# Optimization experiments

Measured on AMD Instinct MI355X. Metric: run time of the kernel, lower is better.

Reference implementation:

```python
import jax, jax.numpy as jnp
import numpy as np
from jax import lax

B, T, FEAT = 8, 512, 128
D_MODEL, D_STATE, D_INNER, DT_RANK = 128, 16, 256, 8
N_LAYERS, NUM_CLASSES = 10, 35
FLAT = 64 * (FEAT // 4)  # 2048


def setup_inputs():
    keys = iter(jax.random.split(jax.random.key(0), 48))
    def nrm(shape, s=0.05):
        return jax.random.normal(next(keys), shape, jnp.float32) * s
    inp = {}
    inp['x'] = jax.random.normal(next(keys), (B, T, FEAT), jnp.float32)
    inp['lengths'] = jax.random.randint(next(keys), (B,), 0, T)
    inp['conv_w1'] = nrm((32, 1, 3, 3)); inp['conv_b1'] = nrm((32,))
    inp['bn1_s'] = 1.0 + nrm((32,)); inp['bn1_b'] = nrm((32,))
    inp['conv_w2'] = nrm((32, 32, 3, 3)); inp['conv_b2'] = nrm((32,))
    inp['bn2_s'] = 1.0 + nrm((32,)); inp['bn2_b'] = nrm((32,))
    inp['conv_w3'] = nrm((64, 32, 3, 3)); inp['conv_b3'] = nrm((64,))
    inp['bn3_s'] = 1.0 + nrm((64,)); inp['bn3_b'] = nrm((64,))
    inp['conv_w4'] = nrm((64, 64, 3, 3)); inp['conv_b4'] = nrm((64,))
    inp['bn4_s'] = 1.0 + nrm((64,)); inp['bn4_b'] = nrm((64,))
    inp['proj_w'] = nrm((D_MODEL, FLAT), 0.02); inp['proj_b'] = nrm((D_MODEL,))
    inp['proj_ln_s'] = jnp.ones((D_MODEL,)); inp['proj_ln_b'] = jnp.zeros((D_MODEL,))
    L = N_LAYERS
    inp['blk_ln_s'] = jnp.ones((L, D_MODEL)); inp['blk_ln_b'] = jnp.zeros((L, D_MODEL))
    inp['in_w'] = nrm((L, 2 * D_INNER, D_MODEL))
    inp['cw'] = nrm((L, D_INNER, 4)); inp['cb'] = nrm((L, D_INNER))
    inp['xp_w'] = nrm((L, DT_RANK + 2 * D_STATE, D_INNER))
    inp['dt_w'] = nrm((L, D_INNER, DT_RANK))
    inp['dt_b'] = nrm((L, D_INNER)) - 4.0  # softplus(-4) ~ 0.018: realistic small dt
    inp['A_log'] = jnp.tile(jnp.log(jnp.arange(1, D_STATE + 1, dtype=jnp.float32))[None, None, :], (L, D_INNER, 1))
    inp['Dp'] = jnp.ones((L, D_INNER))
    inp['out_w'] = nrm((L, D_MODEL, D_INNER))
    inp['pre_ln_s'] = jnp.ones((D_MODEL,)); inp['pre_ln_b'] = jnp.zeros((D_MODEL,))
    inp['cls_w1'] = nrm((D_MODEL // 2, D_MODEL)); inp['cls_b1'] = nrm((D_MODEL // 2,))
    inp['cls_w2'] = nrm((NUM_CLASSES, D_MODEL // 2)); inp['cls_b2'] = nrm((NUM_CLASSES,))
    return inp


def _ln(x, s, b):
    m = jnp.mean(x, -1, keepdims=True)
    v = jnp.mean((x - m) ** 2, -1, keepdims=True)
    return (x - m) * lax.rsqrt(v + 1e-5) * s + b


def _conv2d(x, w, b):
    y = lax.conv_general_dilated(x, w, (1, 1), 'SAME', dimension_numbers=('NCHW', 'OIHW', 'NCHW'))
    return y + b[None, :, None, None]


def _bn(x, s, b):  # eval-mode BatchNorm folded to per-channel affine
    return x * s[None, :, None, None] + b[None, :, None, None]


def _pool(x, kh, kw):
    return lax.reduce_window(x, -jnp.inf, lax.max, (1, 1, kh, kw), (1, 1, kh, kw), 'VALID')


def _mamba(x, in_w, cw, cb, xp_w, dt_w, dt_b, A_log, Dp, out_w):
    bb = x.shape[0]
    xz = jnp.einsum('btd,ed->bte', x, in_w)                  # [B,T,2*d_inner]
    xm, z = jnp.split(xz, 2, axis=-1)
    # causal depthwise conv1d (torch pads both sides by 3 then truncates to T == left-pad 3)
    xc = lax.conv_general_dilated(xm.transpose(0, 2, 1), cw[:, None, :], (1,), [(3, 0)],
                                  dimension_numbers=('NCH', 'OIH', 'NCH'), feature_group_count=D_INNER)
    xc = jax.nn.silu(xc + cb[None, :, None]).transpose(0, 2, 1)  # [B,T,d_inner]
    dbc = jnp.einsum('btd,ed->bte', xc, xp_w)
    dt, Bm, Cm = jnp.split(dbc, [DT_RANK, DT_RANK + D_STATE], axis=-1)
    dt = jax.nn.softplus(jnp.einsum('btr,dr->btd', dt, dt_w) + dt_b)  # [B,T,d_inner]
    A = -jnp.exp(A_log)                                      # [d_inner,d_state]
    dA = jnp.exp(dt[..., None] * A)                          # [B,T,d,n]
    dBu = (dt * xc)[..., None] * Bm[:, :, None, :]           # [B,T,d,n]
    def step(h, inp):
        dA_t, dBu_t, C_t = inp
        h = dA_t * h + dBu_t
        return h, jnp.einsum('bdn,bn->bd', h, C_t)
    h0 = jnp.zeros((bb, D_INNER, D_STATE), x.dtype)
    _, ys = lax.scan(step, h0, (dA.transpose(1, 0, 2, 3), dBu.transpose(1, 0, 2, 3), Cm.transpose(1, 0, 2)))
    y = ys.transpose(1, 0, 2) + Dp * xc
    y = y * jax.nn.silu(z)
    return jnp.einsum('btd,ed->bte', y, out_w)


def _forward(x, lengths, conv_w1, conv_b1, bn1_s, bn1_b, conv_w2, conv_b2, bn2_s, bn2_b,
             conv_w3, conv_b3, bn3_s, bn3_b, conv_w4, conv_b4, bn4_s, bn4_b,
             proj_w, proj_b, proj_ln_s, proj_ln_b, blk_ln_s, blk_ln_b,
             in_w, cw, cb, xp_w, dt_w, dt_b, A_log, Dp, out_w,
             pre_ln_s, pre_ln_b, cls_w1, cls_b1, cls_w2, cls_b2):
    h = x.transpose(0, 2, 1)[:, None]                        # [B,1,F,T]
    h = jax.nn.silu(_bn(_conv2d(h, conv_w1, conv_b1), bn1_s, bn1_b))
    h = jax.nn.silu(_bn(_conv2d(h, conv_w2, conv_b2), bn2_s, bn2_b))
    h = _pool(h, 2, 2)
    h = jax.nn.silu(_bn(_conv2d(h, conv_w3, conv_b3), bn3_s, bn3_b))
    h = jax.nn.silu(_bn(_conv2d(h, conv_w4, conv_b4), bn4_s, bn4_b))
    h = _pool(h, 2, 1)                                       # [B,64,F/4,T/2]
    h = h.transpose(0, 3, 1, 2).reshape(h.shape[0], h.shape[3], -1)  # [B,T',64*F/4]
    h = jax.nn.silu(_ln(jnp.einsum('btf,df->btd', h, proj_w) + proj_b, proj_ln_s, proj_ln_b))
    for i in range(N_LAYERS):
        h = h + _mamba(_ln(h, blk_ln_s[i], blk_ln_b[i]), in_w[i], cw[i], cb[i], xp_w[i],
                       dt_w[i], dt_b[i], A_log[i], Dp[i], out_w[i])
    h = _ln(h, pre_ln_s, pre_ln_b)
    t_lens = jnp.clip(lengths // 2, 1)
    mask = (jnp.arange(h.shape[1])[None, :] < t_lens[:, None]).astype(h.dtype)[..., None]
    pooled = (h * mask).sum(1) / jnp.clip(mask.sum(1), 1.0)
    c = jax.nn.silu(jnp.einsum('bd,hd->bh', pooled, cls_w1) + cls_b1)
    return jnp.einsum('bh,ch->bc', c, cls_w2) + cls_b2


def reference(x, lengths, conv_w1, conv_b1, bn1_s, bn1_b, conv_w2, conv_b2, bn2_s, bn2_b,
              conv_w3, conv_b3, bn3_s, bn3_b, conv_w4, conv_b4, bn4_s, bn4_b,
              proj_w, proj_b, proj_ln_s, proj_ln_b, blk_ln_s, blk_ln_b,
              in_w, cw, cb, xp_w, dt_w, dt_b, A_log, Dp, out_w,
              pre_ln_s, pre_ln_b, cls_w1, cls_b1, cls_w2, cls_b2):
    return _forward(x, lengths, conv_w1, conv_b1, bn1_s, bn1_b, conv_w2, conv_b2, bn2_s, bn2_b,
                    conv_w3, conv_b3, bn3_s, bn3_b, conv_w4, conv_b4, bn4_s, bn4_b,
                    proj_w, proj_b, proj_ln_s, proj_ln_b, blk_ln_s, blk_ln_b,
                    in_w, cw, cb, xp_w, dt_w, dt_b, A_log, Dp, out_w,
                    pre_ln_s, pre_ln_b, cls_w1, cls_b1, cls_w2, cls_b2)
```

## Files before the change

kernel.cpp:

```cpp
#include <hip/hip_runtime.h>
#include <math.h>

#define B_ 8
#define T_ 512
#define FEAT_ 128
#define TP 256
#define DM 128
#define DI 256
#define DS 16
#define DTR 8
#define NL 10

__device__ __forceinline__ float fsilu(float x){ return x / (1.f + __expf(-x)); }
__device__ __forceinline__ float fsoftplus(float x){ return (x > 20.f) ? x : log1pf(__expf(x)); }

template<int CTRL>
__device__ __forceinline__ float dpp_ror(float x){
  int v = __builtin_amdgcn_update_dpp(0, __float_as_int(x), CTRL, 0xF, 0xF, false);
  return __int_as_float(v);
}
__device__ __forceinline__ float rsum16(float x){
  x += dpp_ror<0x121>(x);
  x += dpp_ror<0x122>(x);
  x += dpp_ror<0x124>(x);
  x += dpp_ror<0x128>(x);
  return x;
}

__global__ void k_transpose_x(const float* __restrict__ x, float* __restrict__ xT){
  int idx = blockIdx.x*256 + threadIdx.x;
  if(idx >= B_*FEAT_*T_) return;
  int t = idx % T_; int f = (idx/T_) % FEAT_; int b = idx/(T_*FEAT_);
  xT[idx] = x[((size_t)b*T_ + t)*FEAT_ + f];
}

__device__ __forceinline__ void wt_one(const float* __restrict__ w, float* __restrict__ o,
                                       int idx, int CO, int CIN){
  int k = idx % 9; int ci = (idx/9) % CIN; int co = idx/(9*CIN);
  o[((size_t)(ci*(CO>>3) + (co>>3)))*72 + (co&7)*9 + k] = w[idx];
}
__global__ void k_wt_all(const float* __restrict__ w1, const float* __restrict__ w2,
                         const float* __restrict__ w3, const float* __restrict__ w4,
                         float* __restrict__ o1, float* __restrict__ o2,
                         float* __restrict__ o3, float* __restrict__ o4){
  int idx = blockIdx.x*256 + threadIdx.x;
  if(idx < 288){ wt_one(w1, o1, idx, 32, 1); return; }
  idx -= 288;
  if(idx < 9216){ wt_one(w2, o2, idx, 32, 32); return; }
  idx -= 9216;
  if(idx < 18432){ wt_one(w3, o3, idx, 64, 32); return; }
  idx -= 18432;
  if(idx < 36864){ wt_one(w4, o4, idx, 64, 64); return; }
}

template<int CIN, int CO, int CPW, int CIG, int COG>
__global__ __launch_bounds__(256) void k_conv_t4(const float* __restrict__ in,
     const float* __restrict__ wt, const float* __restrict__ cb,
     const float* __restrict__ bs, const float* __restrict__ bb,
     float* __restrict__ out, int H, int W){
  constexpr int NS = CO/CPW;
  __shared__ __align__(16) float tile[CIG*360];
  int tid = threadIdx.x;
  int lane = tid & 63;
  int wav = __builtin_amdgcn_readfirstlane(tid >> 6);
  int wpr = W >> 4, hpr = H >> 4;
  int idx = blockIdx.x;
  int cog = idx % COG; idx /= COG;
  int tj = idx % wpr; idx /= wpr;
  int ti = idx % hpr; int b = idx / hpr;
  int i0 = ti*16, j0 = tj*16;
  int r = lane & 15, cg = lane >> 4;
  int wslot = cog*4 + wav;
  const float* wbase = wt + (size_t)wslot*72;
  float acc[CPW][4] = {};
  for(int cig = 0; cig < CIN; cig += CIG){
    __syncthreads();
    for(int u = tid; u < CIG*324; u += 256){
      int ci = u / 324; int rem = u - ci*324; int rr = rem / 18; int cc = rem - rr*18;
      int gi = i0 - 1 + rr, gj = j0 - 1 + cc;
      float v = 0.f;
      if(gi >= 0 && gi < H && gj >= 0 && gj < W)
        v = in[((size_t)(b*CIN + cig + ci)*H + gi)*W + gj];
      tile[ci*360 + rr*20 + cc] = v;
    }
    __syncthreads();
    for(int ci = 0; ci < CIG; ci++){
      const float4* wp4 = (const float4*)(wbase + (size_t)(cig+ci)*(NS*72));
      float4 w4q[18];
      #pragma unroll
      for(int q=0;q<18;q++) w4q[q] = wp4[q];
      const float* wf = (const float*)w4q;
      #pragma unroll
      for(int kh=0;kh<3;kh++){
        float4 a = *(const float4*)&tile[ci*360 + (r+kh)*20 + cg*4];
        float4 bv = *(const float4*)&tile[ci*360 + (r+kh)*20 + cg*4 + 4];
        float v[6] = {a.x,a.y,a.z,a.w,bv.x,bv.y};
        #pragma unroll
        for(int co=0;co<CPW;co++){
          #pragma unroll
          for(int kw=0;kw<3;kw++){
            float wv = wf[co*9 + kh*3 + kw];
            #pragma unroll
            for(int u2=0;u2<4;u2++)
              acc[co][u2] = fmaf(wv, v[kw+u2], acc[co][u2]);
          }
        }
      }
    }
  }
  int i = i0 + r;
  #pragma unroll
  for(int co=0; co<CPW; co++){
    int c = cog*(4*CPW) + wav*CPW + co;
    float s = bs[c], bias = cb[c]*s + bb[c];
    float4 o;
    o.x = fsilu(acc[co][0]*s + bias);
    o.y = fsilu(acc[co][1]*s + bias);
    o.z = fsilu(acc[co][2]*s + bias);
    o.w = fsilu(acc[co][3]*s + bias);
    *(float4*)&out[((size_t)(b*CO + c)*H + i)*W + j0 + cg*4] = o;
  }
}

__global__ void k_pool2x2(const float* __restrict__ in, float* __restrict__ out,
                          int C, int Hi, int Wi){
  int Ho = Hi>>1, Wo = Wi>>1;
  int total = B_*C*Ho*Wo;
  int idx = blockIdx.x*256 + threadIdx.x;
  if(idx >= total) return;
  int j = idx % Wo; int i = (idx/Wo)%Ho; int c = (idx/(Wo*Ho))%C; int b = idx/(Wo*Ho*C);
  const float* p = in + (((size_t)(b*C+c)*Hi + 2*i)*Wi + 2*j);
  out[idx] = fmaxf(fmaxf(p[0], p[1]), fmaxf(p[Wi], p[Wi+1]));
}

__global__ __launch_bounds__(256) void k_proj(const float* __restrict__ R0,
    const float* __restrict__ W, float* __restrict__ pbuf){
  __shared__ __align__(16) float As[16][33];
  __shared__ __align__(16) float Ws[16][68];
  int tid = threadIdx.x;
  int n0 = blockIdx.x*64, m0 = blockIdx.y*32;
  int kc = blockIdx.z;
  int b = m0 >> 8;
  int t_base = m0 & 255;
  int tx = tid&15, ty = tid>>4;
  float acc[2][4] = {};
  for(int k0=0; k0<256; k0+=16){
    int kg0 = kc*256 + k0;
    if(tid < 128){
      int row = tid>>2, cq = (tid&3)*4;
      #pragma unroll
      for(int c2=0;c2<4;c2++){
        int k = kg0 + cq + c2;
        int c = k>>5, hh = k&31;
        const float* p = R0 + (((size_t)(b*64+c)*64 + 2*hh)*256 + t_base + row);
        As[cq+c2][row] = fmaxf(p[0], p[256]);
      }
    } else {
      int u = tid - 128; int n = u>>1, cq = (u&1)*8;
      const float* wp = W + (size_t)(n0+n)*2048 + kg0 + cq;
      float4 v0 = *(const float4*)wp, v1 = *(const float4*)(wp+4);
      Ws[cq+0][n]=v0.x; Ws[cq+1][n]=v0.y; Ws[cq+2][n]=v0.z; Ws[cq+3][n]=v0.w;
      Ws[cq+4][n]=v1.x; Ws[cq+5][n]=v1.y; Ws[cq+6][n]=v1.z; Ws[cq+7][n]=v1.w;
    }
    __syncthreads();
    #pragma unroll
    for(int kk=0;kk<16;kk++){
      float a0 = As[kk][ty*2+0];
      float a1 = As[kk][ty*2+1];
      float4 w4 = *(const float4*)&Ws[kk][tx*4];
      float wv4[4] = {w4.x,w4.y,w4.z,w4.w};
      #pragma unroll
      for(int j=0;j<4;j++){
        acc[0][j] = fmaf(a0, wv4[j], acc[0][j]);
        acc[1][j] = fmaf(a1, wv4[j], acc[1][j]);
      }
    }
    __syncthreads();
  }
  float* pb = pbuf + (size_t)kc*2048*DM;
  #pragma unroll
  for(int iu=0;iu<2;iu++){
    int m = m0 + ty*2 + iu;
    #pragma unroll
    for(int j=0;j<4;j++){
      int n = n0 + tx*4 + j;
      pb[(size_t)m*DM + n] = acc[iu][j];
    }
  }
}

__global__ void k_lnp(const float* __restrict__ pbuf, const float* __restrict__ bias,
                      const float* __restrict__ g, const float* __restrict__ b,
                      float* __restrict__ out){
  int row = blockIdx.x;
  int t = threadIdx.x;
  float v0 = bias[t], v1 = bias[t+64];
  #pragma unroll
  for(int kc=0;kc<8;kc++){
    const float* p = pbuf + ((size_t)kc*2048 + row)*DM;
    v0 += p[t]; v1 += p[t+64];
  }
  float s = v0 + v1;
  #pragma unroll
  for(int m=32;m>=1;m>>=1) s += __shfl_xor(s, m);
  float mean = s * (1.f/128.f);
  float e0 = v0-mean, e1 = v1-mean;
  float q = e0*e0 + e1*e1;
  #pragma unroll
  for(int m=32;m>=1;m>>=1) q += __shfl_xor(q, m);
  float inv = rsqrtf(q*(1.f/128.f) + 1e-5f);
  float o0 = fsilu(e0*inv*g[t] + b[t]);
  float o1 = fsilu(e1*inv*g[t+64] + b[t+64]);
  float* po = out + (size_t)row*DM;
  po[t] = o0; po[t+64] = o1;
}

template<int SILU>
__global__ void k_ln(const float* __restrict__ in, const float* __restrict__ g,
                     const float* __restrict__ b, float* __restrict__ out){
  int row = blockIdx.x;
  int t = threadIdx.x;
  const float* p = in + (size_t)row*DM;
  float v0 = p[t], v1 = p[t+64];
  float s = v0 + v1;
  #pragma unroll
  for(int m=32;m>=1;m>>=1) s += __shfl_xor(s, m);
  float mean = s * (1.f/128.f);
  float e0 = v0-mean, e1 = v1-mean;
  float q = e0*e0 + e1*e1;
  #pragma unroll
  for(int m=32;m>=1;m>>=1) q += __shfl_xor(q, m);
  float inv = rsqrtf(q*(1.f/128.f) + 1e-5f);
  float o0 = e0*inv*g[t] + b[t];
  float o1 = e1*inv*g[t+64] + b[t+64];
  if(SILU){ o0 = fsilu(o0); o1 = fsilu(o1); }
  float* po = out + (size_t)row*DM;
  po[t] = o0; po[t+64] = o1;
}

__global__ __launch_bounds__(256) void k_lnxz(const float* __restrict__ hbuf,
    const float* __restrict__ g, const float* __restrict__ bb,
    const float* __restrict__ W, float* __restrict__ out){
  __shared__ __align__(16) float lns[32][132];
  __shared__ __align__(16) float Ws[16][68];
  int tid = threadIdx.x;
  int n0 = blockIdx.x*64, m0 = blockIdx.y*32;
  for(int u=tid; u<1024; u+=256){
    int row = u>>5, c4 = (u&31)*4;
    float4 v = *(const float4*)(hbuf + (size_t)(m0+row)*DM + c4);
    lns[row][c4] = v.x; lns[row][c4+1] = v.y; lns[row][c4+2] = v.z; lns[row][c4+3] = v.w;
  }
  __syncthreads();
  {
    int lane = tid & 63, wv = tid >> 6;
    for(int rr = wv; rr < 32; rr += 4){
      float v0 = lns[rr][lane], v1 = lns[rr][lane+64];
      float s = v0+v1;
      #pragma unroll
      for(int mm=32;mm>=1;mm>>=1) s += __shfl_xor(s,mm);
      float mean = s*(1.f/128.f);
      float e0 = v0-mean, e1 = v1-mean;
      float q = e0*e0+e1*e1;
      #pragma unroll
      for(int mm=32;mm>=1;mm>>=1) q += __shfl_xor(q,mm);
      float inv = rsqrtf(q*(1.f/128.f)+1e-5f);
      lns[rr][lane]    = e0*inv*g[lane] + bb[lane];
      lns[rr][lane+64] = e1*inv*g[lane+64] + bb[lane+64];
    }
  }
  __syncthreads();
  int tx = tid&15, ty = tid>>4;
  float acc[2][4] = {};
  for(int k0=0;k0<128;k0+=16){
    {
      int n = tid>>2, c4 = (tid&3)*4;
      float4 v = *(const float4*)(W + (size_t)(n0+n)*DM + k0 + c4);
      Ws[c4+0][n]=v.x; Ws[c4+1][n]=v.y; Ws[c4+2][n]=v.z; Ws[c4+3][n]=v.w;
    }
    __syncthreads();
    #pragma unroll
    for(int kk=0;kk<16;kk++){
      float a0 = lns[ty*2+0][k0+kk];
      float a1 = lns[ty*2+1][k0+kk];
      float4 w4 = *(const float4*)&Ws[kk][tx*4];
      float wv4[4] = {w4.x,w4.y,w4.z,w4.w};
      #pragma unroll
      for(int j=0;j<4;j++){
        acc[0][j] = fmaf(a0, wv4[j], acc[0][j]);
        acc[1][j] = fmaf(a1, wv4[j], acc[1][j]);
      }
    }
    __syncthreads();
  }
  #pragma unroll
  for(int iu=0;iu<2;iu++){
    int m = m0 + ty*2 + iu;
    float* po = out + (size_t)m*512 + n0 + tx*4;
    #pragma unroll
    for(int j=0;j<4;j++) po[j] = acc[iu][j];
  }
}

__global__ __launch_bounds__(256) void k_xproj8(const float* __restrict__ xz,
    const float* __restrict__ cw, const float* __restrict__ cb,
    const float* __restrict__ xpw, const float* __restrict__ dtw,
    const float* __restrict__ dtb_, float* __restrict__ xc_g,
    float* __restrict__ dbc_g, float* __restrict__ dt_g){
  __shared__ float xzs[11][64];
  __shared__ float As[64][9];
  __shared__ float Wp[64][41];
  __shared__ float dtin[8][9];
  __shared__ float dtw_s[256][9];
  int tid = threadIdx.x;
  int row0 = blockIdx.x*8; int b = row0 >> 8; int t0 = row0 & 255;
  int rA = tid & 7, cgA = tid >> 3;
  int dlC = tid & 63, rqC = tid >> 6;
  float acc0 = 0.f, acc1 = 0.f;
  for(int ch=0; ch<4; ch++){
    int d0 = ch*64;
    __syncthreads();
    for(int u=tid; u<11*64; u+=256){
      int rr = u>>6, dl = u&63;
      int t = t0 + rr - 3;
      xzs[rr][dl] = (t >= 0) ? xz[((size_t)(b*TP)+t)*512 + d0 + dl] : 0.f;
    }
    for(int u=tid; u<40*64; u+=256){
      int nn = u>>6, dk = u&63;
      Wp[dk][nn] = xpw[(size_t)nn*DI + d0 + dk];
    }
    __syncthreads();
    {
      float cw0 = cw[(d0+dlC)*4+0], cw1 = cw[(d0+dlC)*4+1];
      float cw2 = cw[(d0+dlC)*4+2], cw3 = cw[(d0+dlC)*4+3];
      float cbv = cb[d0+dlC];
      #pragma unroll
      for(int i=0;i<2;i++){
        int rr = rqC*2 + i;
        float a = cbv;
        a = fmaf(cw0, xzs[rr+0][dlC], a);
        a = fmaf(cw1, xzs[rr+1][dlC], a);
        a = fmaf(cw2, xzs[rr+2][dlC], a);
        a = fmaf(cw3, xzs[rr+3][dlC], a);
        float v = fsilu(a);
        As[dlC][rr] = v;
        xc_g[((size_t)row0 + rr)*DI + d0 + dlC] = v;
      }
    }
    __syncthreads();
    for(int dk=0; dk<64; dk++){
      float a = As[dk][rA];
      acc0 = fmaf(a, Wp[dk][cgA], acc0);
      if(cgA < 8) acc1 = fmaf(a, Wp[dk][cgA+32], acc1);
    }
  }
  if(cgA < 8){
    dtin[rA][cgA] = acc0;
    dbc_g[((size_t)row0 + rA)*40 + cgA + 32] = acc1;
  } else {
    dbc_g[((size_t)row0 + rA)*40 + cgA] = acc0;
  }
  for(int u=tid; u<256*8; u+=256) dtw_s[u>>3][u&7] = dtw[u];
  __syncthreads();
  {
    int d = tid;
    float bias = dtb_[d];
    float w8[8];
    #pragma unroll
    for(int k=0;k<8;k++) w8[k] = dtw_s[d][k];
    #pragma unroll
    for(int r2=0;r2<8;r2++){
      float a = bias;
      #pragma unroll
      for(int k=0;k<8;k++) a = fmaf(dtin[r2][k], w8[k], a);
      dt_g[((size_t)row0 + r2)*DI + d] = fsoftplus(a);
    }
  }
}

__global__ __launch_bounds__(1024) void k_scan4(const float* __restrict__ dtb,
      const float* __restrict__ xc, const float* __restrict__ xz,
      const float* __restrict__ dbc, const float* __restrict__ A_log,
      const float* __restrict__ Dp, float* __restrict__ y){
  __shared__ float dt_s[TP][8], xc_s[TP][8];
  __shared__ float Bs[TP][16], Cs[TP][16];
  __shared__ float Eb[8][128], Pb[8][128];
  int tid = threadIdx.x;
  int c = tid >> 7, gl = (tid >> 4) & 7, n = tid & 15;
  int dblk = blockIdx.x & 31, b = blockIdx.x >> 5;
  int d0 = dblk*8;
  size_t rbase = (size_t)b*TP;
  for(int u=tid; u<TP*8; u+=1024){
    int tt = u>>3, gg = u&7;
    size_t r = rbase + tt;
    dt_s[tt][gg] = dtb[r*DI + d0 + gg];
    xc_s[tt][gg] = xc [r*DI + d0 + gg];
  }
  for(int u=tid; u<TP*16; u+=1024){
    int tt = u>>4, nn = u&15;
    size_t r = rbase + tt;
    Bs[tt][nn] = dbc[r*40 + 8  + nn];
    Cs[tt][nn] = dbc[r*40 + 24 + nn];
  }
  __syncthreads();
  int d = d0 + gl;
  float An = -__expf(A_log[d*DS + n]);
  float h = 0.f, dtsum = 0.f;
  int tA = c*32;
  float hc[32], ev[32];
  #pragma unroll
  for(int i=0;i<32;i++){
    int t = tA + i;
    float dtv = dt_s[t][gl];
    dtsum += dtv;
    float e = __expf(dtv*An);
    ev[i] = e;
    h = fmaf(e, h, dtv*xc_s[t][gl]*Bs[t][n]);
    hc[i] = h*Cs[t][n];
  }
  Eb[c][gl*16+n] = h;
  Pb[c][gl*16+n] = __expf(An*dtsum);
  __syncthreads();
  float g = 0.f;
  for(int cp=0; cp<c; cp++)
    g = fmaf(Pb[cp][gl*16+n], g, Eb[cp][gl*16+n]);
  float Dpd = Dp[d];
  #pragma unroll
  for(int i=0;i<32;i++){
    int t = tA + i;
    g *= ev[i];
    float p = rsum16(hc[i] + g*Cs[t][n]);
    if(n==0){
      float zv = xz[(rbase+t)*512 + DI + d];
      float xcv = xc_s[t][gl];
      y[(rbase+t)*DI + d] = (p + Dpd*xcv) * fsilu(zv);
    }
  }
}

__global__ __launch_bounds__(256) void k_out16(const float* __restrict__ A,
    const float* __restrict__ W, float* __restrict__ C){
  __shared__ float As[16][17];
  __shared__ __align__(16) float Ws[16][68];
  int tid = threadIdx.x;
  int n0 = blockIdx.x*64, m0 = blockIdx.y*16;
  int tx = tid&15, ty = tid>>4;
  float acc[4] = {};
  for(int k0=0;k0<256;k0+=16){
    {
      int row = tid>>4, kk = tid&15;
      As[kk][row] = A[(size_t)(m0+row)*DI + k0 + kk];
    }
    {
      int n = tid>>2, cq = (tid&3)*4;
      float4 v = *(const float4*)(W + (size_t)(n0+n)*DI + k0 + cq);
      Ws[cq+0][n]=v.x; Ws[cq+1][n]=v.y; Ws[cq+2][n]=v.z; Ws[cq+3][n]=v.w;
    }
    __syncthreads();
    #pragma unroll
    for(int kk=0;kk<16;kk++){
      float a0 = As[kk][ty];
      float4 w4 = *(const float4*)&Ws[kk][tx*4];
      acc[0] = fmaf(a0, w4.x, acc[0]);
      acc[1] = fmaf(a0, w4.y, acc[1]);
      acc[2] = fmaf(a0, w4.z, acc[2]);
      acc[3] = fmaf(a0, w4.w, acc[3]);
    }
    __syncthreads();
  }
  int m = m0 + ty;
  float* cp = &C[(size_t)m*DM + n0 + tx*4];
  cp[0] += acc[0]; cp[1] += acc[1]; cp[2] += acc[2]; cp[3] += acc[3];
}

__global__ void k_head(const float* __restrict__ hln, const int* __restrict__ lengths,
                       const float* __restrict__ w1, const float* __restrict__ b1,
                       const float* __restrict__ w2, const float* __restrict__ b2,
                       float* __restrict__ out){
  __shared__ float pooled[DM];
  __shared__ float cbuf[64];
  int b = blockIdx.x, tid = threadIdx.x;
  int tl = lengths[b] >> 1; if(tl < 1) tl = 1;
  float s = 0.f;
  const float* p = hln + (size_t)b*TP*DM + tid;
  for(int t=0;t<tl;t++) s += p[(size_t)t*DM];
  pooled[tid] = s / (float)tl;
  __syncthreads();
  if(tid < 64){
    float a = b1[tid];
    const float* wp = w1 + tid*DM;
    for(int k=0;k<DM;k++) a = fmaf(pooled[k], wp[k], a);
    cbuf[tid] = fsilu(a);
  }
  __syncthreads();
  if(tid < 35){
    float a = b2[tid];
    const float* wp = w2 + tid*64;
    for(int k=0;k<64;k++) a = fmaf(cbuf[k], wp[k], a);
    out[b*35+tid] = a;
  }
}

extern "C" void kernel_launch(void* const* d_in, const int* in_sizes, int n_in,
                              void* d_out, int out_size, void* d_ws, size_t ws_size,
                              hipStream_t stream){
  (void)in_sizes; (void)n_in; (void)out_size; (void)ws_size;
  const float* x        = (const float*)d_in[0];
  const int*   lengths  = (const int*)  d_in[1];
  const float* conv_w1  = (const float*)d_in[2];  const float* conv_b1 = (const float*)d_in[3];
  const float* bn1_s    = (const float*)d_in[4];  const float* bn1_b   = (const float*)d_in[5];
  const float* conv_w2  = (const float*)d_in[6];  const float* conv_b2 = (const float*)d_in[7];
  const float* bn2_s    = (const float*)d_in[8];  const float* bn2_b   = (const float*)d_in[9];
  const float* conv_w3  = (const float*)d_in[10]; const float* conv_b3 = (const float*)d_in[11];
  const float* bn3_s    = (const float*)d_in[12]; const float* bn3_b   = (const float*)d_in[13];
  const float* conv_w4  = (const float*)d_in[14]; const float* conv_b4 = (const float*)d_in[15];
  const float* bn4_s    = (const float*)d_in[16]; const float* bn4_b   = (const float*)d_in[17];
  const float* proj_w   = (const float*)d_in[18]; const float* proj_b  = (const float*)d_in[19];
  const float* proj_ln_s= (const float*)d_in[20]; const float* proj_ln_b=(const float*)d_in[21];
  const float* blk_ln_s = (const float*)d_in[22]; const float* blk_ln_b =(const float*)d_in[23];
  const float* in_w     = (const float*)d_in[24];
  const float* cw       = (const float*)d_in[25]; const float* cbv     = (const float*)d_in[26];
  const float* xp_w     = (const float*)d_in[27];
  const float* dt_w     = (const float*)d_in[28]; const float* dt_b    = (const float*)d_in[29];
  const float* A_log    = (const float*)d_in[30]; const float* Dp      = (const float*)d_in[31];
  const float* out_w    = (const float*)d_in[32];
  const float* pre_ln_s = (const float*)d_in[33]; const float* pre_ln_b= (const float*)d_in[34];
  const float* cls_w1   = (const float*)d_in[35]; const float* cls_b1  = (const float*)d_in[36];
  const float* cls_w2   = (const float*)d_in[37]; const float* cls_b2  = (const float*)d_in[38];

  float* ws   = (float*)d_ws;
  float* R0   = ws;
  float* R1   = R0 + 16777216;
  float* xT   = R1 + 16777216;
  float* hbuf = xT + 524288;
  float* lnb  = hbuf + 262144;
  float* xzb  = lnb + 262144;
  float* xcb  = xzb + 1048576;
  float* dbcb = xcb + 524288;
  float* dtbb = dbcb + 81920;
  float* yb   = dtbb + 524288;
  float* wt1  = yb + 524288;
  float* wt2  = wt1 + 288;
  float* wt3  = wt2 + 9216;
  float* wt4  = wt3 + 18432;

  k_wt_all<<<254, 256, 0, stream>>>(conv_w1, conv_w2, conv_w3, conv_w4, wt1, wt2, wt3, wt4);

  k_transpose_x<<<2048, 256, 0, stream>>>(x, xT);
  k_conv_t4<1,32,8,1,1><<<8*8*32, 256, 0, stream>>>(xT, wt1, conv_b1, bn1_s, bn1_b, R0, 128, 512);
  k_conv_t4<32,32,8,8,1><<<8*8*32, 256, 0, stream>>>(R0, wt2, conv_b2, bn2_s, bn2_b, R1, 128, 512);
  k_pool2x2<<<(8*32*64*256)/256, 256, 0, stream>>>(R1, R0, 32, 128, 512);
  k_conv_t4<32,64,8,8,2><<<8*4*16*2, 256, 0, stream>>>(R0, wt3, conv_b3, bn3_s, bn3_b, R1, 64, 256);
  k_conv_t4<64,64,8,8,2><<<8*4*16*2, 256, 0, stream>>>(R1, wt4, conv_b4, bn4_s, bn4_b, R0, 64, 256);

  {
    dim3 gd(2, 64, 8);
    k_proj<<<gd, 256, 0, stream>>>(R0, proj_w, R1);
  }
  k_lnp<<<2048, 64, 0, stream>>>(R1, proj_b, proj_ln_s, proj_ln_b, hbuf);

  for(int i=0;i<NL;i++){
    { dim3 gd(8, 64);
      k_lnxz<<<gd, 256, 0, stream>>>(hbuf, blk_ln_s + i*DM, blk_ln_b + i*DM,
                                     in_w + (size_t)i*512*DM, xzb); }
    k_xproj8<<<256, 256, 0, stream>>>(xzb, cw + (size_t)i*DI*4, cbv + i*DI,
                                      xp_w + (size_t)i*40*DI, dt_w + (size_t)i*DI*DTR,
                                      dt_b + i*DI, xcb, dbcb, dtbb);
    k_scan4<<<256, 1024, 0, stream>>>(dtbb, xcb, xzb, dbcb, A_log + (size_t)i*DI*DS, Dp + i*DI, yb);
    { dim3 gd(2, 128);
      k_out16<<<gd, 256, 0, stream>>>(yb, out_w + (size_t)i*DM*DI, hbuf); }
  }

  k_ln<0><<<2048, 64, 0, stream>>>(hbuf, pre_ln_s, pre_ln_b, lnb);
  k_head<<<8, 128, 0, stream>>>(lnb, lengths, cls_w1, cls_b1, cls_w2, cls_b2, (float*)d_out);
}
```

Baseline: 1.198 ms.

## Use packed fp16 dot2 accumulation for conv layers 2-4

Conv layers 2-4 now pack pairs of input channels into fp16x2 in the shared tile and in the pre-transposed weights, and accumulate with v_dot2 into fp32. This halves the FMA instruction count, shared-memory tile size and weight register loads per input channel pair. In exchange, activations and weights lose precision to fp16, and the tile fill now does two strided global loads plus a conversion per element.

Result: faster. 1.154 ms (-3.6%).

```diff
diff --git a/kernel.cpp b/kernel.cpp
--- a/kernel.cpp
+++ b/kernel.cpp
@@ -11,8 +11,20 @@
 #define DTR 8
 #define NL 10
 
+typedef _Float16 h2 __attribute__((ext_vector_type(2)));
+typedef unsigned int uint32;
+
 __device__ __forceinline__ float fsilu(float x){ return x / (1.f + __expf(-x)); }
 __device__ __forceinline__ float fsoftplus(float x){ return (x > 20.f) ? x : log1pf(__expf(x)); }
+
+__device__ __forceinline__ uint32 pack_h2(float a, float b){
+  union { h2 h; uint32 u; } cv;
+  cv.h[0] = (_Float16)a; cv.h[1] = (_Float16)b;
+  return cv.u;
+}
+__device__ __forceinline__ h2 as_h2(uint32 u){
+  union { uint32 u; h2 h; } cv; cv.u = u; return cv.h;
+}
 
 template<int CTRL>
 __device__ __forceinline__ float dpp_ror(float x){
@@ -39,18 +51,26 @@
   int k = idx % 9; int ci = (idx/9) % CIN; int co = idx/(9*CIN);
   o[((size_t)(ci*(CO>>3) + (co>>3)))*72 + (co&7)*9 + k] = w[idx];
 }
+__device__ __forceinline__ void wt_pack(const float* __restrict__ w, uint32* __restrict__ o,
+                                        int idx, int CO, int CIN){
+  int CIN2 = CIN >> 1;
+  int k = idx % 9; int ci2 = (idx/9) % CIN2; int co = idx/(9*CIN2);
+  float f0 = w[((size_t)co*CIN + 2*ci2 + 0)*9 + k];
+  float f1 = w[((size_t)co*CIN + 2*ci2 + 1)*9 + k];
+  o[((size_t)(ci2*(CO>>3) + (co>>3)))*72 + (co&7)*9 + k] = pack_h2(f0, f1);
+}
 __global__ void k_wt_all(const float* __restrict__ w1, const float* __restrict__ w2,
                          const float* __restrict__ w3, const float* __restrict__ w4,
-                         float* __restrict__ o1, float* __restrict__ o2,
-                         float* __restrict__ o3, float* __restrict__ o4){
+                         float* __restrict__ o1, uint32* __restrict__ o2,
+                         uint32* __restrict__ o3, uint32* __restrict__ o4){
   int idx = blockIdx.x*256 + threadIdx.x;
   if(idx < 288){ wt_one(w1, o1, idx, 32, 1); return; }
   idx -= 288;
-  if(idx < 9216){ wt_one(w2, o2, idx, 32, 32); return; }
+  if(idx < 4608){ wt_pack(w2, o2, idx, 32, 32); return; }
+  idx -= 4608;
+  if(idx < 9216){ wt_pack(w3, o3, idx, 64, 32); return; }
   idx -= 9216;
-  if(idx < 18432){ wt_one(w3, o3, idx, 64, 32); return; }
-  idx -= 18432;
-  if(idx < 36864){ wt_one(w4, o4, idx, 64, 64); return; }
+  if(idx < 18432){ wt_pack(w4, o4, idx, 64, 64); return; }
 }
 
 template<int CIN, int CO, int CPW, int CIG, int COG>
@@ -103,6 +123,84 @@
             #pragma unroll
             for(int u2=0;u2<4;u2++)
               acc[co][u2] = fmaf(wv, v[kw+u2], acc[co][u2]);
+          }
+        }
+      }
+    }
+  }
+  int i = i0 + r;
+  #pragma unroll
+  for(int co=0; co<CPW; co++){
+    int c = cog*(4*CPW) + wav*CPW + co;
+    float s = bs[c], bias = cb[c]*s + bb[c];
+    float4 o;
+    o.x = fsilu(acc[co][0]*s + bias);
+    o.y = fsilu(acc[co][1]*s + bias);
+    o.z = fsilu(acc[co][2]*s + bias);
+    o.w = fsilu(acc[co][3]*s + bias);
+    *(float4*)&out[((size_t)(b*CO + c)*H + i)*W + j0 + cg*4] = o;
+  }
+}
+
+template<int CIN2, int CO, int CPW, int CIG2, int COG>
+__global__ __launch_bounds__(256) void k_conv_t7(const float* __restrict__ in,
+     const uint32* __restrict__ wt, const float* __restrict__ cb,
+     const float* __restrict__ bs, const float* __restrict__ bb,
+     float* __restrict__ out, int H, int W){
+  constexpr int NS = CO/CPW;
+  __shared__ __align__(16) uint32 tile[CIG2*360];
+  int tid = threadIdx.x;
+  int lane = tid & 63;
+  int wav = __builtin_amdgcn_readfirstlane(tid >> 6);
+  int wpr = W >> 4, hpr = H >> 4;
+  int idx = blockIdx.x;
+  int cog = idx % COG; idx /= COG;
+  int tj = idx % wpr; idx /= wpr;
+  int ti = idx % hpr; int b = idx / hpr;
+  int i0 = ti*16, j0 = tj*16;
+  int r = lane & 15, cg = lane >> 4;
+  int wslot = cog*4 + wav;
+  const uint32* wbase = wt + (size_t)wslot*72;
+  float acc[CPW][4] = {};
+  for(int c2g = 0; c2g < CIN2; c2g += CIG2){
+    __syncthreads();
+    for(int u = tid; u < CIG2*324; u += 256){
+      int ci2 = u / 324; int rem = u - ci2*324; int rr = rem / 18; int cc = rem - rr*18;
+      int gi = i0 - 1 + rr, gj = j0 - 1 + cc;
+      float v0 = 0.f, v1 = 0.f;
+      if(gi >= 0 && gi < H && gj >= 0 && gj < W){
+        const float* p = in + ((size_t)(b*(CIN2*2) + (c2g+ci2)*2)*H + gi)*W + gj;
+        v0 = p[0];
+        v1 = p[(size_t)H*W];
+      }
+      tile[ci2*360 + rr*20 + cc] = pack_h2(v0, v1);
+    }
+    __syncthreads();
+    for(int ci2 = 0; ci2 < CIG2; ci2++){
+      const uint4* wp4 = (const uint4*)(wbase + (size_t)(c2g+ci2)*(NS*72));
+      uint4 w4q[18];
+      #pragma unroll
+      for(int q=0;q<18;q++) w4q[q] = wp4[q];
+      const uint32* wf = (const uint32*)w4q;
+      h2 v[3][6];
+      #pragma unroll
+      for(int kh=0;kh<3;kh++){
+        const uint32* trow = &tile[ci2*360 + (r+kh)*20 + cg*4];
+        uint4 a4 = *(const uint4*)trow;
+        v[kh][0]=as_h2(a4.x); v[kh][1]=as_h2(a4.y);
+        v[kh][2]=as_h2(a4.z); v[kh][3]=as_h2(a4.w);
+        v[kh][4]=as_h2(trow[4]); v[kh][5]=as_h2(trow[5]);
+      }
+      #pragma unroll
+      for(int co=0;co<CPW;co++){
+        #pragma unroll
+        for(int kh=0;kh<3;kh++){
+          #pragma unroll
+          for(int kw=0;kw<3;kw++){
+            h2 wv = as_h2(wf[co*9 + kh*3 + kw]);
+            #pragma unroll
+            for(int u2=0;u2<4;u2++)
+              acc[co][u2] = __builtin_amdgcn_fdot2(wv, v[kh][kw+u2], acc[co][u2], false);
           }
         }
       }
@@ -539,18 +637,19 @@
   float* dtbb = dbcb + 81920;
   float* yb   = dtbb + 524288;
   float* wt1  = yb + 524288;
-  float* wt2  = wt1 + 288;
-  float* wt3  = wt2 + 9216;
-  float* wt4  = wt3 + 18432;
-
-  k_wt_all<<<254, 256, 0, stream>>>(conv_w1, conv_w2, conv_w3, conv_w4, wt1, wt2, wt3, wt4);
+  uint32* wt2h = (uint32*)(wt1 + 288);
+  uint32* wt3h = wt2h + 4608;
+  uint32* wt4h = wt3h + 9216;
+
+  k_wt_all<<<128, 256, 0, stream>>>(conv_w1, conv_w2, conv_w3, conv_w4,
+                                    wt1, wt2h, wt3h, wt4h);
 
   k_transpose_x<<<2048, 256, 0, stream>>>(x, xT);
   k_conv_t4<1,32,8,1,1><<<8*8*32, 256, 0, stream>>>(xT, wt1, conv_b1, bn1_s, bn1_b, R0, 128, 512);
-  k_conv_t4<32,32,8,8,1><<<8*8*32, 256, 0, stream>>>(R0, wt2, conv_b2, bn2_s, bn2_b, R1, 128, 512);
+  k_conv_t7<16,32,8,4,1><<<8*8*32, 256, 0, stream>>>(R0, wt2h, conv_b2, bn2_s, bn2_b, R1, 128, 512);
   k_pool2x2<<<(8*32*64*256)/256, 256, 0, stream>>>(R1, R0, 32, 128, 512);
-  k_conv_t4<32,64,8,8,2><<<8*4*16*2, 256, 0, stream>>>(R0, wt3, conv_b3, bn3_s, bn3_b, R1, 64, 256);
-  k_conv_t4<64,64,8,8,2><<<8*4*16*2, 256, 0, stream>>>(R1, wt4, conv_b4, bn4_s, bn4_b, R0, 64, 256);
+  k_conv_t7<16,64,8,4,2><<<8*4*16*2, 256, 0, stream>>>(R0, wt3h, conv_b3, bn3_s, bn3_b, R1, 64, 256);
+  k_conv_t7<32,64,8,4,2><<<8*4*16*2, 256, 0, stream>>>(R1, wt4h, conv_b4, bn4_s, bn4_b, R0, 64, 256);
 
   {
     dim3 gd(2, 64, 8);
```
